# Kernel tuning notes

Measured on AMD Instinct MI355X. Metric: run time of the kernel, lower is better.

The kernel has to match this reference:

```python
import jax, jax.numpy as jnp
import numpy as np

NUM_HEADS = 16


def setup_inputs() -> dict:
    B, S, E = 4, 2048, 2048
    key = jax.random.key(0)
    kx, kq, kk, kv, kc = jax.random.split(key, 5)
    sc = 1.0 / np.sqrt(E).astype(np.float32)
    return {
        "x": jax.random.normal(kx, (B, S, E), dtype=jnp.float32),
        # Linear weights stored as [in, out] (equivalent to torch W.T)
        "Wq": jax.random.normal(kq, (E, E), dtype=jnp.float32) * sc,
        "bq": jnp.zeros((E,), dtype=jnp.float32),
        "Wk": jax.random.normal(kk, (E, E), dtype=jnp.float32) * sc,
        "bk": jnp.zeros((E,), dtype=jnp.float32),
        "Wv": jax.random.normal(kv, (E, E), dtype=jnp.float32) * sc,
        "bv": jnp.zeros((E,), dtype=jnp.float32),
        "Wc": jax.random.normal(kc, (E, E), dtype=jnp.float32) * sc,
        "bc": jnp.zeros((E,), dtype=jnp.float32),
    }


def reference(x, Wq, bq, Wk, bk, Wv, bv, Wc, bc):
    B, S, E = x.shape
    H = NUM_HEADS
    d = E // H
    q = (x @ Wq + bq).reshape(B, S, H, d)
    k = (x @ Wk + bk).reshape(B, S, H, d)
    v = (x @ Wv + bv).reshape(B, S, H, d)
    # full O(S^2) score matrix, scaled by 1/sqrt(head_dim)
    att = jnp.einsum("bihd,bjhd->bhij", q, k) * (1.0 / np.sqrt(d).astype(np.float32))
    causal = jnp.tril(jnp.ones((S, S), dtype=bool))
    att = jnp.where(causal[None, None, :, :], att, -jnp.inf)
    att = jax.nn.softmax(att, axis=-1)
    # NOTE: faithful to source einsum 'bhij,bihd->bihd' (sums attn over j,
    # broadcasts v over i), i.e. y = v * rowsum(att) == v since rows sum to 1.
    y = jnp.einsum("bhij,bihd->bihd", att, v).reshape(B, S, E)
    return y @ Wc + bc
```

## Files before the change

kernel.cpp:

```cpp
#include <hip/hip_runtime.h>

#define ED 2048
#define MR 8192

typedef unsigned short u16;
typedef _Float16 f16;
typedef __attribute__((ext_vector_type(8))) __bf16 bf16x8;
typedef __attribute__((ext_vector_type(8))) _Float16 f16x8;
typedef __attribute__((ext_vector_type(4))) float f32x4;

__device__ __forceinline__ u16 f2bf(float f){ __bf16 h=(__bf16)f; return __builtin_bit_cast(u16,h); }
__device__ __forceinline__ float bf2f(u16 u){ __bf16 h=__builtin_bit_cast(__bf16,u); return (float)h; }

#define MFMA16 __builtin_amdgcn_mfma_f32_16x16x32_f16
#define MFMAB  __builtin_amdgcn_mfma_f32_16x16x32_bf16

#define LDSLOAD(gp, lp) __builtin_amdgcn_global_load_lds( \
    (const __attribute__((address_space(1))) unsigned int*)(gp), \
    (__attribute__((address_space(3))) unsigned int*)(lp), 16, 0, 0)

__global__ void cast16(const float* __restrict__ in, f16* __restrict__ out, int n8) {
    int i = blockIdx.x * 256 + threadIdx.x;
    const int stride = gridDim.x * 256;
    for (; i < n8; i += stride) {
        float4 a = reinterpret_cast<const float4*>(in)[2 * i];
        float4 b = reinterpret_cast<const float4*>(in)[2 * i + 1];
        f16x8 v;
        v[0] = (f16)a.x; v[1] = (f16)a.y; v[2] = (f16)a.z; v[3] = (f16)a.w;
        v[4] = (f16)b.x; v[5] = (f16)b.y; v[6] = (f16)b.z; v[7] = (f16)b.w;
        *reinterpret_cast<f16x8*>(out + (size_t)i * 8) = v;
    }
}

__global__ void transpose_f16(const float* __restrict__ in, f16* __restrict__ out, int n) {
    __shared__ float tile[32][33];
    const int bx = blockIdx.x * 32, by = blockIdx.y * 32;
    const int tx = threadIdx.x & 31, ty = threadIdx.x >> 5;
    #pragma unroll
    for (int r = ty; r < 32; r += 8)
        tile[r][tx] = in[(size_t)(by + r) * n + bx + tx];
    __syncthreads();
    #pragma unroll
    for (int r = ty; r < 32; r += 8)
        out[(size_t)(bx + r) * n + by + tx] = (f16)tile[tx][r];
}

__global__ void transpose_f32(const float* __restrict__ in, float* __restrict__ out, int n) {
    __shared__ float tile[32][33];
    const int bx = blockIdx.x * 32, by = blockIdx.y * 32;
    const int tx = threadIdx.x & 31, ty = threadIdx.x >> 5;
    #pragma unroll
    for (int r = ty; r < 32; r += 8)
        tile[r][tx] = in[(size_t)(by + r) * n + bx + tx];
    __syncthreads();
    #pragma unroll
    for (int r = ty; r < 32; r += 8)
        out[(size_t)(bx + r) * n + by + tx] = tile[tx][r];
}

__global__ void split_kernel(const float* __restrict__ in, u16* __restrict__ hi,
                             u16* __restrict__ lo, int n4) {
    int i = blockIdx.x * 256 + threadIdx.x;
    const int stride = gridDim.x * 256;
    for (; i < n4; i += stride) {
        float4 v = reinterpret_cast<const float4*>(in)[i];
        ushort4 h, l;
        h.x = f2bf(v.x); l.x = f2bf(v.x - bf2f(h.x));
        h.y = f2bf(v.y); l.y = f2bf(v.y - bf2f(h.y));
        h.z = f2bf(v.z); l.z = f2bf(v.z - bf2f(h.z));
        h.w = f2bf(v.w); l.w = f2bf(v.w - bf2f(h.w));
        reinterpret_cast<ushort4*>(hi)[i] = h;
        reinterpret_cast<ushort4*>(lo)[i] = l;
    }
}

__global__ void bias_kernel(const float* __restrict__ bv, const float* __restrict__ Wc,
                            const float* __restrict__ bc, float* __restrict__ bp) {
    const int n = blockIdx.x * 256 + threadIdx.x;
    const int j0 = blockIdx.y * 64;
    float s = (blockIdx.y == 0) ? bc[n] : 0.0f;
    #pragma unroll 4
    for (int j = 0; j < 64; ++j)
        s += bv[j0 + j] * Wc[(size_t)(j0 + j) * ED + n];
    atomicAdd(&bp[n], s);
}

__global__ __launch_bounds__(512, 1)
void gemm256f(const f16* __restrict__ A, const f16* __restrict__ B,
              float* __restrict__ Cout, const float* __restrict__ bias,
              int Kd, int Nd)
{
    __shared__ __align__(16) f16 sA[2][8192];
    __shared__ __align__(16) f16 sB[2][8192];

    const int tid = threadIdx.x, lane = tid & 63, wave = tid >> 6;
    const int wm = wave >> 2, wn = wave & 3;
    const int lrow = lane & 15, kq = lane >> 4;

    const int nwg = gridDim.x * gridDim.y;
    const int lin = blockIdx.y * gridDim.x + blockIdx.x;
    const int lin2 = (lin & 7) * (nwg >> 3) + (lin >> 3);
    const int bx = lin2 % gridDim.x, by = lin2 / gridDim.x;
    const long m0 = (long)bx * 256;
    const long n0 = (long)by * 256;

    const int c0 = wave * 2, c1 = c0 + 1;
    const int lb0 = c0 * 512, lb1 = c1 * 512;
    const long ga0 = (m0 + (c0 & 3) * 64 + lane) * (long)Kd + (c0 >> 2) * 8;
    const long ga1 = (m0 + (c1 & 3) * 64 + lane) * (long)Kd + (c1 >> 2) * 8;
    const long gb0 = (n0 + (c0 & 3) * 64 + lane) * (long)Kd + (c0 >> 2) * 8;
    const long gb1 = (n0 + (c1 & 3) * 64 + lane) * (long)Kd + (c1 >> 2) * 8;

    f32x4 acc[8][4];
    #pragma unroll
    for (int i = 0; i < 8; ++i)
        #pragma unroll
        for (int j = 0; j < 4; ++j)
            acc[i][j] = (f32x4){0.f, 0.f, 0.f, 0.f};

#define STAGE(buf, kt) do { \
    LDSLOAD(A + ga0 + (kt), &sA[buf][lb0]); \
    LDSLOAD(A + ga1 + (kt), &sA[buf][lb1]); \
    LDSLOAD(B + gb0 + (kt), &sB[buf][lb0]); \
    LDSLOAD(B + gb1 + (kt), &sB[buf][lb1]); \
} while (0)

    const int NT = Kd >> 5;
    STAGE(0, 0);

    for (int t = 0; t < NT; ++t) {
        const int cur = t & 1;
        if (t + 1 < NT) {
            STAGE(cur ^ 1, (t + 1) << 5);
            asm volatile("s_waitcnt vmcnt(4)" ::: "memory");
        } else {
            asm volatile("s_waitcnt vmcnt(0)" ::: "memory");
        }
        __builtin_amdgcn_s_barrier();
        __builtin_amdgcn_sched_barrier(0);

        f16x8 bf[4];
        #pragma unroll
        for (int fn = 0; fn < 4; ++fn) {
            int off = kq * 2048 + (wn * 64 + fn * 16 + lrow) * 8;
            bf[fn] = *reinterpret_cast<const f16x8*>(&sB[cur][off]);
        }
        #pragma unroll
        for (int fm = 0; fm < 8; ++fm) {
            int off = kq * 2048 + (wm * 128 + fm * 16 + lrow) * 8;
            f16x8 af = *reinterpret_cast<const f16x8*>(&sA[cur][off]);
            #pragma unroll
            for (int fn = 0; fn < 4; ++fn)
                acc[fm][fn] = MFMA16(af, bf[fn], acc[fm][fn], 0, 0, 0);
        }

        __builtin_amdgcn_sched_barrier(0);
        __builtin_amdgcn_s_barrier();
    }
#undef STAGE

    #pragma unroll
    for (int fm = 0; fm < 8; ++fm) {
        long gmb = m0 + wm * 128 + fm * 16 + kq * 4;
        #pragma unroll
        for (int fn = 0; fn < 4; ++fn) {
            long gn = n0 + wn * 64 + fn * 16 + lrow;
            float bb = bias[gn];
            #pragma unroll
            for (int i = 0; i < 4; ++i)
                Cout[(gmb + i) * Nd + gn] = acc[fm][fn][i] + bb;
        }
    }
}

__global__ __launch_bounds__(256, 2)
void gemmW16(const f16* __restrict__ A, const f16* __restrict__ B,
             f16* __restrict__ Cout, int Kd, int Nd)
{
    __shared__ __align__(16) f16 sA[2][4096];
    __shared__ __align__(16) f16 sB[2][4096];

    const int tid = threadIdx.x, lane = tid & 63, wave = tid >> 6;
    const int wm = wave >> 1, wn = wave & 1;
    const int lrow = lane & 15, kq = lane >> 4;

    const int nwg = gridDim.x * gridDim.y;
    const int lin = blockIdx.y * gridDim.x + blockIdx.x;
    const int lin2 = (lin & 7) * (nwg >> 3) + (lin >> 3);
    const int bx = lin2 % gridDim.x, by = lin2 / gridDim.x;
    const long m0 = (long)bx * 128;
    const long n0 = (long)by * 128;

    const int c0 = wave * 2, c1 = c0 + 1;
    const int lb0 = c0 * 512, lb1 = c1 * 512;
    const long ga0 = (m0 + (c0 & 1) * 64 + lane) * (long)Kd + (c0 >> 1) * 8;
    const long ga1 = (m0 + (c1 & 1) * 64 + lane) * (long)Kd + (c1 >> 1) * 8;
    const long gb0 = (n0 + (c0 & 1) * 64 + lane) * (long)Kd + (c0 >> 1) * 8;
    const long gb1 = (n0 + (c1 & 1) * 64 + lane) * (long)Kd + (c1 >> 1) * 8;

    f32x4 acc[4][4];
    #pragma unroll
    for (int i = 0; i < 4; ++i)
        #pragma unroll
        for (int j = 0; j < 4; ++j)
            acc[i][j] = (f32x4){0.f, 0.f, 0.f, 0.f};

#define STAGEW(buf, kt) do { \
    LDSLOAD(A + ga0 + (kt), &sA[buf][lb0]); \
    LDSLOAD(A + ga1 + (kt), &sA[buf][lb1]); \
    LDSLOAD(B + gb0 + (kt), &sB[buf][lb0]); \
    LDSLOAD(B + gb1 + (kt), &sB[buf][lb1]); \
} while (0)

    const int NT = Kd >> 5;
    STAGEW(0, 0);

    for (int t = 0; t < NT; ++t) {
        const int cur = t & 1;
        if (t + 1 < NT) {
            STAGEW(cur ^ 1, (t + 1) << 5);
            asm volatile("s_waitcnt vmcnt(4)" ::: "memory");
        } else {
            asm volatile("s_waitcnt vmcnt(0)" ::: "memory");
        }
        __builtin_amdgcn_s_barrier();
        __builtin_amdgcn_sched_barrier(0);

        f16x8 bf[4];
        #pragma unroll
        for (int fn = 0; fn < 4; ++fn) {
            int off = kq * 1024 + (wn * 64 + fn * 16 + lrow) * 8;
            bf[fn] = *reinterpret_cast<const f16x8*>(&sB[cur][off]);
        }
        #pragma unroll
        for (int fm = 0; fm < 4; ++fm) {
            int off = kq * 1024 + (wm * 64 + fm * 16 + lrow) * 8;
            f16x8 af = *reinterpret_cast<const f16x8*>(&sA[cur][off]);
            #pragma unroll
            for (int fn = 0; fn < 4; ++fn)
                acc[fm][fn] = MFMA16(af, bf[fn], acc[fm][fn], 0, 0, 0);
        }

        __builtin_amdgcn_sched_barrier(0);
        __builtin_amdgcn_s_barrier();
    }
#undef STAGEW

    #pragma unroll
    for (int fm = 0; fm < 4; ++fm) {
        long gmb = m0 + wm * 64 + fm * 16 + kq * 4;
        #pragma unroll
        for (int fn = 0; fn < 4; ++fn) {
            long gn = n0 + wn * 64 + fn * 16 + lrow;
            #pragma unroll
            for (int i = 0; i < 4; ++i)
                Cout[(gmb + i) * Nd + gn] = (f16)acc[fm][fn][i];
        }
    }
}

template<int EPIL, int APRE, int BPRE>
__global__ __launch_bounds__(256)
void gemm3(const float* __restrict__ Af, const u16* __restrict__ Ahi, const u16* __restrict__ Alo,
           const float* __restrict__ Btf, const u16* __restrict__ Bhi, const u16* __restrict__ Blo,
           float* __restrict__ Cout, const float* __restrict__ bias,
           u16* __restrict__ Ohi, u16* __restrict__ Olo, int Kd, int Ld, int Nd)
{
    __shared__ __align__(16) u16 sAhi[4096];
    __shared__ __align__(16) u16 sAlo[4096];
    __shared__ __align__(16) u16 sBhi[4096];
    __shared__ __align__(16) u16 sBlo[4096];

    const int tid = threadIdx.x, lane = tid & 63, wave = tid >> 6;
    const int wm = wave >> 1, wn = wave & 1;
    const int lrow = lane & 15, kq = lane >> 4;

    const int nwg = gridDim.x * gridDim.y;
    const int lin = blockIdx.y * gridDim.x + blockIdx.x;
    const int lin2 = (lin & 7) * (nwg >> 3) + (lin >> 3);
    const int bx = lin2 % gridDim.x, by = lin2 / gridDim.x;
    const long m0 = (long)bx * 128;
    const long n0 = (long)by * 128;
    const long koff = (long)blockIdx.z * Kd;
    if (EPIL == 2) Cout += (size_t)blockIdx.z * (size_t)gridDim.x * 128 * Nd;

    const int idx0 = wave * 2, idx1 = wave * 2 + 1;
    const int s0 = idx0 & 3, h0 = idx0 >> 2;
    const int s1 = idx1 & 3, h1 = idx1 >> 2;
    const int cb0 = s0 * 1024 + h0 * 512;
    const int cb1 = s1 * 1024 + h1 * 512;
    const long ga0 = (m0 + h0 * 64 + lane) * (long)Ld + koff + s0 * 8;
    const long ga1 = (m0 + h1 * 64 + lane) * (long)Ld + koff + s1 * 8;
    const long gb0 = (n0 + h0 * 64 + lane) * (long)Ld + koff + s0 * 8;
    const long gb1 = (n0 + h1 * 64 + lane) * (long)Ld + koff + s1 * 8;

    f32x4 acc[4][4];
    #pragma unroll
    for (int i = 0; i < 4; ++i)
        #pragma unroll
        for (int j = 0; j < 4; ++j)
            acc[i][j] = (f32x4){0.f, 0.f, 0.f, 0.f};

    float4 av[4], bvv[4];
    if (!APRE) {
        #pragma unroll
        for (int i = 0; i < 4; ++i) {
            int ch = tid + i * 256, r = ch >> 3, c4 = ch & 7;
            av[i] = *reinterpret_cast<const float4*>(Af + (m0 + r) * (long)Ld + koff + c4 * 4);
        }
    }
    if (!BPRE) {
        #pragma unroll
        for (int i = 0; i < 4; ++i) {
            int ch = tid + i * 256, r = ch >> 3, c4 = ch & 7;
            bvv[i] = *reinterpret_cast<const float4*>(Btf + (n0 + r) * (long)Ld + koff + c4 * 4);
        }
    }

    for (int kt = 0; kt < Kd; kt += 32) {
        if (APRE) {
            LDSLOAD(Ahi + ga0 + kt, sAhi + cb0);
            LDSLOAD(Ahi + ga1 + kt, sAhi + cb1);
            LDSLOAD(Alo + ga0 + kt, sAlo + cb0);
            LDSLOAD(Alo + ga1 + kt, sAlo + cb1);
        } else {
            #pragma unroll
            for (int i = 0; i < 4; ++i) {
                int ch = tid + i * 256, r = ch >> 3, c4 = ch & 7;
                int off = (c4 >> 1) * 1024 + r * 8 + (c4 & 1) * 4;
                ushort4 h, l;
                h.x = f2bf(av[i].x); l.x = f2bf(av[i].x - bf2f(h.x));
                h.y = f2bf(av[i].y); l.y = f2bf(av[i].y - bf2f(h.y));
                h.z = f2bf(av[i].z); l.z = f2bf(av[i].z - bf2f(h.z));
                h.w = f2bf(av[i].w); l.w = f2bf(av[i].w - bf2f(h.w));
                *reinterpret_cast<ushort4*>(&sAhi[off]) = h;
                *reinterpret_cast<ushort4*>(&sAlo[off]) = l;
            }
        }
        if (BPRE) {
            LDSLOAD(Bhi + gb0 + kt, sBhi + cb0);
            LDSLOAD(Bhi + gb1 + kt, sBhi + cb1);
            LDSLOAD(Blo + gb0 + kt, sBlo + cb0);
            LDSLOAD(Blo + gb1 + kt, sBlo + cb1);
        } else {
            #pragma unroll
            for (int i = 0; i < 4; ++i) {
                int ch = tid + i * 256, r = ch >> 3, c4 = ch & 7;
                int off = (c4 >> 1) * 1024 + r * 8 + (c4 & 1) * 4;
                ushort4 h, l;
                h.x = f2bf(bvv[i].x); l.x = f2bf(bvv[i].x - bf2f(h.x));
                h.y = f2bf(bvv[i].y); l.y = f2bf(bvv[i].y - bf2f(h.y));
                h.z = f2bf(bvv[i].z); l.z = f2bf(bvv[i].z - bf2f(h.z));
                h.w = f2bf(bvv[i].w); l.w = f2bf(bvv[i].w - bf2f(h.w));
                *reinterpret_cast<ushort4*>(&sBhi[off]) = h;
                *reinterpret_cast<ushort4*>(&sBlo[off]) = l;
            }
        }

        __syncthreads();

        if (!APRE && kt + 32 < Kd) {
            #pragma unroll
            for (int i = 0; i < 4; ++i) {
                int ch = tid + i * 256, r = ch >> 3, c4 = ch & 7;
                av[i] = *reinterpret_cast<const float4*>(Af + (m0 + r) * (long)Ld + koff + kt + 32 + c4 * 4);
            }
        }
        if (!BPRE && kt + 32 < Kd) {
            #pragma unroll
            for (int i = 0; i < 4; ++i) {
                int ch = tid + i * 256, r = ch >> 3, c4 = ch & 7;
                bvv[i] = *reinterpret_cast<const float4*>(Btf + (n0 + r) * (long)Ld + koff + kt + 32 + c4 * 4);
            }
        }

        bf16x8 bh[4], bl[4];
        #pragma unroll
        for (int fn = 0; fn < 4; ++fn) {
            int r = wn * 64 + fn * 16 + lrow;
            bh[fn] = *reinterpret_cast<const bf16x8*>(&sBhi[kq * 1024 + r * 8]);
            bl[fn] = *reinterpret_cast<const bf16x8*>(&sBlo[kq * 1024 + r * 8]);
        }
        #pragma unroll
        for (int fm = 0; fm < 4; ++fm) {
            int r = wm * 64 + fm * 16 + lrow;
            bf16x8 ah = *reinterpret_cast<const bf16x8*>(&sAhi[kq * 1024 + r * 8]);
            bf16x8 al = *reinterpret_cast<const bf16x8*>(&sAlo[kq * 1024 + r * 8]);
            #pragma unroll
            for (int fn = 0; fn < 4; ++fn) {
                acc[fm][fn] = MFMAB(ah, bh[fn], acc[fm][fn], 0, 0, 0);
                acc[fm][fn] = MFMAB(ah, bl[fn], acc[fm][fn], 0, 0, 0);
                acc[fm][fn] = MFMAB(al, bh[fn], acc[fm][fn], 0, 0, 0);
            }
        }

        __syncthreads();
    }

    #pragma unroll
    for (int fm = 0; fm < 4; ++fm) {
        long gmb = m0 + wm * 64 + fm * 16 + kq * 4;
        #pragma unroll
        for (int fn = 0; fn < 4; ++fn) {
            long gn = n0 + wn * 64 + fn * 16 + lrow;
            float bb = (EPIL == 0) ? bias[gn] : 0.0f;
            #pragma unroll
            for (int i = 0; i < 4; ++i) {
                float w = acc[fm][fn][i];
                if (EPIL == 0) {
                    Cout[(gmb + i) * Nd + gn] = w + bb;
                } else if (EPIL == 2) {
                    Cout[(gmb + i) * Nd + gn] = w;
                } else {
                    u16 h = f2bf(w);
                    Ohi[(gmb + i) * Nd + gn] = h;
                    Olo[(gmb + i) * Nd + gn] = f2bf(w - bf2f(h));
                }
            }
        }
    }
}

extern "C" void kernel_launch(void* const* d_in, const int* in_sizes, int n_in,
                              void* d_out, int out_size, void* d_ws, size_t ws_size,
                              hipStream_t stream) {
    const float* x  = (const float*)d_in[0];
    const float* Wv = (const float*)d_in[5];
    const float* bv = (const float*)d_in[6];
    const float* Wc = (const float*)d_in[7];
    const float* bc = (const float*)d_in[8];
    float* out = (float*)d_out;

    char* ws = (char*)d_ws;
    const size_t MB = 1024 * 1024;

    float* bp = (float*)ws;
    hipMemsetAsync(bp, 0, ED * sizeof(float), stream);
    bias_kernel<<<dim3(ED / 256, ED / 64), 256, 0, stream>>>(bv, Wc, bc, bp);

    if (ws_size >= 60 * MB + 8192) {
        f16* xh   = (f16*)(ws + 8192);
        f16* Wpt  = (f16*)(ws + 8192 + 32 * MB);
        f16* Wct  = (f16*)(ws + 8192 + 40 * MB);
        f16* Wvh  = (f16*)(ws + 8192 + 48 * MB);

        cast16<<<2048, 256, 0, stream>>>(x, xh, MR * ED / 8);
        transpose_f16<<<dim3(64, 64), 256, 0, stream>>>(Wc, Wct, ED);
        cast16<<<1024, 256, 0, stream>>>(Wv, Wvh, ED * ED / 8);
        gemmW16<<<dim3(16, 16), 256, 0, stream>>>(Wct, Wvh, Wpt, ED, ED);
        gemm256f<<<dim3(MR / 256, ED / 256), 512, 0, stream>>>(
            xh, Wpt, out, bp, ED, ED);
    } else {
        float* Wctf = (float*)(ws + 8192);
        u16* Wpt_hi = (u16*)(ws + 8192 + 16 * MB);
        u16* Wpt_lo = (u16*)(ws + 8192 + 24 * MB);

        transpose_f32<<<dim3(64, 64), 256, 0, stream>>>(Wc, Wctf, ED);
        gemm3<1, 0, 0><<<dim3(16, 16), 256, 0, stream>>>(
            Wctf, nullptr, nullptr, Wv, nullptr, nullptr,
            nullptr, nullptr, Wpt_hi, Wpt_lo, ED, ED, ED);
        gemm3<0, 0, 1><<<dim3(64, 16), 256, 0, stream>>>(
            x, nullptr, nullptr, nullptr, Wpt_hi, Wpt_lo,
            out, bp, nullptr, nullptr, ED, ED, ED);
    }
}
```

Before: 378.1 us.

## Deepen GEMM prefetch to four LDS stages and use 8 waves in weight GEMM

Both f16 GEMMs move from double-buffered to four-stage LDS buffering, keeping three K-tiles of global-to-LDS loads in flight, with matching vmcnt waits. The weight-product GEMM switches from 4 to 8 waves per block, each wave holding a 64x32 sub-tile and issuing one A and one B async load per stage. The main 256x256 GEMM's LDS footprint doubles to 128 KB, which occupancy 1 allows but which may still limit residency. The unused split kernel is removed.

```diff
diff --git a/kernel.cpp b/kernel.cpp
--- a/kernel.cpp
+++ b/kernel.cpp
@@ -58,22 +58,6 @@
         out[(size_t)(bx + r) * n + by + tx] = tile[tx][r];
 }
 
-__global__ void split_kernel(const float* __restrict__ in, u16* __restrict__ hi,
-                             u16* __restrict__ lo, int n4) {
-    int i = blockIdx.x * 256 + threadIdx.x;
-    const int stride = gridDim.x * 256;
-    for (; i < n4; i += stride) {
-        float4 v = reinterpret_cast<const float4*>(in)[i];
-        ushort4 h, l;
-        h.x = f2bf(v.x); l.x = f2bf(v.x - bf2f(h.x));
-        h.y = f2bf(v.y); l.y = f2bf(v.y - bf2f(h.y));
-        h.z = f2bf(v.z); l.z = f2bf(v.z - bf2f(h.z));
-        h.w = f2bf(v.w); l.w = f2bf(v.w - bf2f(h.w));
-        reinterpret_cast<ushort4*>(hi)[i] = h;
-        reinterpret_cast<ushort4*>(lo)[i] = l;
-    }
-}
-
 __global__ void bias_kernel(const float* __restrict__ bv, const float* __restrict__ Wc,
                             const float* __restrict__ bc, float* __restrict__ bp) {
     const int n = blockIdx.x * 256 + threadIdx.x;
@@ -90,8 +74,8 @@
               float* __restrict__ Cout, const float* __restrict__ bias,
               int Kd, int Nd)
 {
-    __shared__ __align__(16) f16 sA[2][8192];
-    __shared__ __align__(16) f16 sB[2][8192];
+    __shared__ __align__(16) f16 sA[4][8192];
+    __shared__ __align__(16) f16 sB[4][8192];
 
     const int tid = threadIdx.x, lane = tid & 63, wave = tid >> 6;
     const int wm = wave >> 2, wn = wave & 3;
@@ -127,11 +111,17 @@
 
     const int NT = Kd >> 5;
     STAGE(0, 0);
+    STAGE(1, 32);
+    STAGE(2, 64);
 
     for (int t = 0; t < NT; ++t) {
-        const int cur = t & 1;
-        if (t + 1 < NT) {
-            STAGE(cur ^ 1, (t + 1) << 5);
+        const int cur = t & 3;
+        if (t + 3 < NT) {
+            STAGE((t + 3) & 3, (t + 3) << 5);
+            asm volatile("s_waitcnt vmcnt(12)" ::: "memory");
+        } else if (t + 2 < NT) {
+            asm volatile("s_waitcnt vmcnt(8)" ::: "memory");
+        } else if (t + 1 < NT) {
             asm volatile("s_waitcnt vmcnt(4)" ::: "memory");
         } else {
             asm volatile("s_waitcnt vmcnt(0)" ::: "memory");
@@ -173,15 +163,15 @@
     }
 }
 
-__global__ __launch_bounds__(256, 2)
+__global__ __launch_bounds__(512, 1)
 void gemmW16(const f16* __restrict__ A, const f16* __restrict__ B,
              f16* __restrict__ Cout, int Kd, int Nd)
 {
-    __shared__ __align__(16) f16 sA[2][4096];
-    __shared__ __align__(16) f16 sB[2][4096];
+    __shared__ __align__(16) f16 sA[4][4096];
+    __shared__ __align__(16) f16 sB[4][4096];
 
     const int tid = threadIdx.x, lane = tid & 63, wave = tid >> 6;
-    const int wm = wave >> 1, wn = wave & 1;
+    const int wm = wave >> 2, wn = wave & 3;
     const int lrow = lane & 15, kq = lane >> 4;
 
     const int nwg = gridDim.x * gridDim.y;
@@ -191,45 +181,46 @@
     const long m0 = (long)bx * 128;
     const long n0 = (long)by * 128;
 
-    const int c0 = wave * 2, c1 = c0 + 1;
-    const int lb0 = c0 * 512, lb1 = c1 * 512;
-    const long ga0 = (m0 + (c0 & 1) * 64 + lane) * (long)Kd + (c0 >> 1) * 8;
-    const long ga1 = (m0 + (c1 & 1) * 64 + lane) * (long)Kd + (c1 >> 1) * 8;
-    const long gb0 = (n0 + (c0 & 1) * 64 + lane) * (long)Kd + (c0 >> 1) * 8;
-    const long gb1 = (n0 + (c1 & 1) * 64 + lane) * (long)Kd + (c1 >> 1) * 8;
-
-    f32x4 acc[4][4];
+    const int lb = (wave >> 1) * 1024 + (wave & 1) * 512;
+    const long ga = (m0 + (wave & 1) * 64 + lane) * (long)Kd + (wave >> 1) * 8;
+    const long gb = (n0 + (wave & 1) * 64 + lane) * (long)Kd + (wave >> 1) * 8;
+
+    f32x4 acc[4][2];
     #pragma unroll
     for (int i = 0; i < 4; ++i)
         #pragma unroll
-        for (int j = 0; j < 4; ++j)
+        for (int j = 0; j < 2; ++j)
             acc[i][j] = (f32x4){0.f, 0.f, 0.f, 0.f};
 
 #define STAGEW(buf, kt) do { \
-    LDSLOAD(A + ga0 + (kt), &sA[buf][lb0]); \
-    LDSLOAD(A + ga1 + (kt), &sA[buf][lb1]); \
-    LDSLOAD(B + gb0 + (kt), &sB[buf][lb0]); \
-    LDSLOAD(B + gb1 + (kt), &sB[buf][lb1]); \
+    LDSLOAD(A + ga + (kt), &sA[buf][lb]); \
+    LDSLOAD(B + gb + (kt), &sB[buf][lb]); \
 } while (0)
 
     const int NT = Kd >> 5;
     STAGEW(0, 0);
+    STAGEW(1, 32);
+    STAGEW(2, 64);
 
     for (int t = 0; t < NT; ++t) {
-        const int cur = t & 1;
-        if (t + 1 < NT) {
-            STAGEW(cur ^ 1, (t + 1) << 5);
+        const int cur = t & 3;
+        if (t + 3 < NT) {
+            STAGEW((t + 3) & 3, (t + 3) << 5);
+            asm volatile("s_waitcnt vmcnt(6)" ::: "memory");
+        } else if (t + 2 < NT) {
             asm volatile("s_waitcnt vmcnt(4)" ::: "memory");
+        } else if (t + 1 < NT) {
+            asm volatile("s_waitcnt vmcnt(2)" ::: "memory");
         } else {
             asm volatile("s_waitcnt vmcnt(0)" ::: "memory");
         }
         __builtin_amdgcn_s_barrier();
         __builtin_amdgcn_sched_barrier(0);
 
-        f16x8 bf[4];
-        #pragma unroll
-        for (int fn = 0; fn < 4; ++fn) {
-            int off = kq * 1024 + (wn * 64 + fn * 16 + lrow) * 8;
+        f16x8 bf[2];
+        #pragma unroll
+        for (int fn = 0; fn < 2; ++fn) {
+            int off = kq * 1024 + (wn * 32 + fn * 16 + lrow) * 8;
             bf[fn] = *reinterpret_cast<const f16x8*>(&sB[cur][off]);
         }
         #pragma unroll
@@ -237,7 +228,7 @@
             int off = kq * 1024 + (wm * 64 + fm * 16 + lrow) * 8;
             f16x8 af = *reinterpret_cast<const f16x8*>(&sA[cur][off]);
             #pragma unroll
-            for (int fn = 0; fn < 4; ++fn)
+            for (int fn = 0; fn < 2; ++fn)
                 acc[fm][fn] = MFMA16(af, bf[fn], acc[fm][fn], 0, 0, 0);
         }
 
@@ -250,8 +241,8 @@
     for (int fm = 0; fm < 4; ++fm) {
         long gmb = m0 + wm * 64 + fm * 16 + kq * 4;
         #pragma unroll
-        for (int fn = 0; fn < 4; ++fn) {
-            long gn = n0 + wn * 64 + fn * 16 + lrow;
+        for (int fn = 0; fn < 2; ++fn) {
+            long gn = n0 + wn * 32 + fn * 16 + lrow;
             #pragma unroll
             for (int i = 0; i < 4; ++i)
                 Cout[(gmb + i) * Nd + gn] = (f16)acc[fm][fn][i];
@@ -447,7 +438,7 @@
         cast16<<<2048, 256, 0, stream>>>(x, xh, MR * ED / 8);
         transpose_f16<<<dim3(64, 64), 256, 0, stream>>>(Wc, Wct, ED);
         cast16<<<1024, 256, 0, stream>>>(Wv, Wvh, ED * ED / 8);
-        gemmW16<<<dim3(16, 16), 256, 0, stream>>>(Wct, Wvh, Wpt, ED, ED);
+        gemmW16<<<dim3(16, 16), 512, 0, stream>>>(Wct, Wvh, Wpt, ED, ED);
         gemm256f<<<dim3(MR / 256, ED / 256), 512, 0, stream>>>(
             xh, Wpt, out, bp, ED, ED);
     } else {
```

Measured after the change: 367.9 us. 1.03x faster.
